# Optimization experiments

Measured on AMD Instinct MI355X. Metric: run time of the kernel, lower is better.

The kernel has to match this reference:

```python
import jax, jax.numpy as jnp
import numpy as np

N = 50000   # total nodes
E = 100000  # total edges
F = 64      # input node features
H = 128     # hidden_dim
HEADS = 4
B = 64      # number of graphs in the batch
S = 512     # num_stations
LC = 8      # num_line_colors


def setup_inputs() -> dict:
    key = jax.random.key(0)
    ks = jax.random.split(key, 40)
    w = lambda i, shape: (jax.random.normal(ks[i], shape, jnp.float32) * 0.02)
    inp = {
        'node_features': jax.random.normal(ks[0], (N, F), jnp.float32),
        'edge_index': jax.random.randint(ks[1], (2, E), 0, N),
        'batch': jnp.sort(jax.random.randint(ks[2], (N,), 0, B)),
        # initial projection F -> H
        'Wp': w(3, (F, H)), 'bp': w(4, (H,)),
        # TransformerConv 1: in H, out H, heads HEADS (concat)
        'Wq1': w(5, (H, HEADS * H)), 'bq1': w(6, (HEADS * H,)),
        'Wk1': w(7, (H, HEADS * H)), 'bk1': w(8, (HEADS * H,)),
        'Wv1': w(9, (H, HEADS * H)), 'bv1': w(10, (HEADS * H,)),
        'Ws1': w(11, (H, HEADS * H)), 'bs1': w(12, (HEADS * H,)),
        # TransformerConv 2: in HEADS*H, out H, heads 1
        'Wq2': w(13, (HEADS * H, H)), 'bq2': w(14, (H,)),
        'Wk2': w(15, (HEADS * H, H)), 'bk2': w(16, (H,)),
        'Wv2': w(17, (HEADS * H, H)), 'bv2': w(18, (H,)),
        'Ws2': w(19, (HEADS * H, H)), 'bs2': w(20, (H,)),
        # output heads
        'crW': w(21, (H, 1)),  'crb': w(22, (1,)),
        'hlW': w(23, (H, 4)),  'hlb': w(24, (4,)),
        'mtW': w(25, (H, 3)),  'mtb': w(26, (3,)),
        'p1W': w(27, (H, S)),  'p1b': w(28, (S,)),
        'p2W': w(29, (H, S)),  'p2b': w(30, (S,)),
        'dtW': w(31, (H, S)),  'dtb': w(32, (S,)),
        'slW': w(33, (H, LC)), 'slb': w(34, (LC,)),
    }
    return inp


def transformer_conv(x, src, dst, Wq, bq, Wk, bk, Wv, bv, Ws, bs, heads, out_ch):
    # PyG TransformerConv (beta=False, concat=True, root_weight=True):
    #   alpha_ij = softmax_j( (W_q x_i) . (W_k x_j) / sqrt(d) ) over in-edges of i
    #   out_i    = sum_j alpha_ij * (W_v x_j)  (concat heads) + W_skip x_i
    n = x.shape[0]
    q = (x @ Wq + bq).reshape(n, heads, out_ch)
    k = (x @ Wk + bk).reshape(n, heads, out_ch)
    v = (x @ Wv + bv).reshape(n, heads, out_ch)
    scores = jnp.sum(q[dst] * k[src], axis=-1) / jnp.sqrt(jnp.float32(out_ch))  # [E,heads]
    m = jax.ops.segment_max(scores, dst, num_segments=n)                        # per-target max
    e = jnp.exp(scores - m[dst])
    denom = jax.ops.segment_sum(e, dst, num_segments=n)
    alpha = e / (denom[dst] + 1e-16)                                            # [E,heads]
    out = jax.ops.segment_sum(alpha[:, :, None] * v[src], dst, num_segments=n)  # [N,heads,out]
    return out.reshape(n, heads * out_ch) + (x @ Ws + bs)


def reference(node_features, edge_index, batch, Wp, bp,
              Wq1, bq1, Wk1, bk1, Wv1, bv1, Ws1, bs1,
              Wq2, bq2, Wk2, bk2, Wv2, bv2, Ws2, bs2,
              crW, crb, hlW, hlb, mtW, mtb, p1W, p1b, p2W, p2b, dtW, dtb, slW, slb):
    src, dst = edge_index[0], edge_index[1]
    h = jax.nn.relu(node_features @ Wp + bp)
    h = jax.nn.relu(transformer_conv(h, src, dst, Wq1, bq1, Wk1, bk1, Wv1, bv1, Ws1, bs1, HEADS, H))
    h = jax.nn.relu(transformer_conv(h, src, dst, Wq2, bq2, Wk2, bk2, Wv2, bv2, Ws2, bs2, 1, H))
    # global mean pool over graphs
    counts = jax.ops.segment_sum(jnp.ones((h.shape[0],), h.dtype), batch, num_segments=B)
    g = jax.ops.segment_sum(h, batch, num_segments=B) / jnp.maximum(counts, 1.0)[:, None]  # [B,H]
    value = g @ crW + crb
    return (value,
            g @ hlW + hlb,
            g @ mtW + mtb,
            g @ p1W + p1b,
            g @ p2W + p2b,
            g @ dtW + dtb,
            g @ slW + slb)
```

## Files before the change

### kernel.cpp

```cpp
#include <hip/hip_runtime.h>
#include <hip/hip_bf16.h>

#define NN 50000
#define EE 100000
#define FF 64
#define HH 128
#define HEADS 4
#define BB 64
#define SS 512
#define LCC 8
#define DEGCAP 32

__device__ __forceinline__ float b2f(ushort u) {
    return __uint_as_float(((unsigned)u) << 16);
}
__device__ __forceinline__ ushort f2b(float f) {
    unsigned u = __float_as_uint(f);
    unsigned r = (u + 0x7FFFu + ((u >> 16) & 1u)) >> 16;
    return (ushort)r;
}
__device__ __forceinline__ uint f2b_pk(float a, float b) {
    __hip_bfloat162 h = __float22bfloat162_rn(make_float2(a, b));
    return *reinterpret_cast<uint*>(&h);
}

__device__ __forceinline__ uint f2fp8x4(float a, float b, float c, float d) {
    int r = __builtin_amdgcn_cvt_pk_fp8_f32(a, b, 0, false);
    r = __builtin_amdgcn_cvt_pk_fp8_f32(c, d, r, true);
    return (uint)r;
}
__device__ __forceinline__ void fp8x4(uint u, float* f) {
    auto lo = __builtin_amdgcn_cvt_pk_f32_fp8((int)u, false);
    auto hi = __builtin_amdgcn_cvt_pk_f32_fp8((int)u, true);
    f[0] = lo[0]; f[1] = lo[1]; f[2] = hi[0]; f[3] = hi[1];
}

typedef __attribute__((ext_vector_type(4))) float f32x4;
typedef __attribute__((ext_vector_type(8))) short s16x8;
typedef __attribute__((ext_vector_type(4))) uint u32x4;

__device__ __forceinline__ void glls16(const ushort* g, ushort* l) {
    __builtin_amdgcn_global_load_lds((const __attribute__((address_space(1))) void*)g,
                                     (__attribute__((address_space(3))) void*)l, 16, 0, 0);
}

#define BM 128
#define BN 128
#define BK 64
#define EST 68

__global__ __launch_bounds__(512) void gemm_wide(
    const ushort* __restrict__ A, const ushort* __restrict__ Bt,
    const float* __restrict__ bias,
    ushort* __restrict__ C1,
    unsigned char* __restrict__ D0, unsigned char* __restrict__ D1,
    unsigned char* __restrict__ D2,
    int mode, int M, int K, int gx, int gy)
{
    __shared__ __align__(16) ushort Sm[384 * 64];

    const int bid  = blockIdx.x;
    const int xcd  = bid & 7;
    const int slot = bid >> 3;
    const int bx   = slot % gx;
    const int by   = xcd + 8 * (slot / gx);
    if (by >= gy) return;
    const int m0 = by * BM;
    const int n0 = bx * 256;

    const int t = threadIdx.x;
    const int lane = t & 63;
    const int wave = t >> 6;
    const int wm = (wave & 1) * 64;
    const int wn = (wave >> 1) * 64;
    const int lrow = lane & 15;
    const int g    = lane >> 4;

    const int wbase = n0 + wn;
    float bj[4];
#pragma unroll
    for (int j = 0; j < 4; ++j) bj[j] = bias[wbase + j * 16 + lrow];

    const int scs = lane & 7;
    const ushort* gp[6];
#pragma unroll
    for (int p = 0; p < 6; ++p) {
        const int row = wave * 48 + p * 8 + (lane >> 3);
        const int l   = scs ^ (row & 7);
        gp[p] = (row < 128)
              ? A  + (size_t)min(m0 + row, M - 1) * K + (l << 3)
              : Bt + (size_t)(n0 + row - 128) * K + (l << 3);
    }

    f32x4 acc[4][4];
#pragma unroll
    for (int i = 0; i < 4; ++i)
#pragma unroll
        for (int j = 0; j < 4; ++j)
            acc[i][j] = (f32x4){bj[j], bj[j], bj[j], bj[j]};

    for (int k0 = 0; k0 < K; k0 += BK) {
#pragma unroll
        for (int p = 0; p < 6; ++p)
            glls16(gp[p] + k0, Sm + (wave * 48 + p * 8) * 64);
        __syncthreads();

#pragma unroll
        for (int kk = 0; kk < 2; ++kk) {
            s16x8 af[4], bf[4];
#pragma unroll
            for (int i = 0; i < 4; ++i) {
                const int R = wm + i * 16 + lrow;
                const int c = ((kk << 2) + g) ^ (R & 7);
                af[i] = *(const s16x8*)&Sm[(R << 6) + (c << 3)];
            }
#pragma unroll
            for (int j = 0; j < 4; ++j) {
                const int R = wn + j * 16 + lrow;
                const int c = ((kk << 2) + g) ^ (R & 7);
                bf[j] = *(const s16x8*)&Sm[((128 + R) << 6) + (c << 3)];
            }
#pragma unroll
            for (int i = 0; i < 4; ++i)
#pragma unroll
                for (int j = 0; j < 4; ++j)
                    acc[i][j] = __builtin_amdgcn_mfma_f32_16x16x32_bf16(af[i], bf[j], acc[i][j], 0, 0, 0);
        }
        __syncthreads();
    }

    float* Es = (float*)Sm + wave * (16 * EST);

    int dsel;
    ushort* Cw = C1; int ldw = 128; int cb = wbase;
    unsigned char* Cw8 = nullptr; int ldw8 = 0, cb8 = 0;
    if (mode == 1) {
        dsel = 1;
        if (wbase < 512) { Cw8 = D0; ldw8 = 512; cb8 = wbase; }
        else {
            const int u = wbase - 512;
            const int h = u >> 8;
            const int c = u & 255;
            if (c < 128) { Cw8 = D1; ldw8 = 512; cb8 = h * 128 + c; }
            else         { Cw8 = D2; ldw8 = 512; cb8 = h * 128 + (c - 128); }
        }
    } else {
        if (wbase < 128) { dsel = 0; }
        else { dsel = 1; Cw8 = D0; ldw8 = 384; cb8 = wbase - 128; }
    }

    const int rbase = (lane >> 4) * 4;
    const int rrow  = lane >> 2;
    const int rcol  = (lane & 3) << 4;

#pragma unroll
    for (int i = 0; i < 4; ++i) {
#pragma unroll
        for (int j = 0; j < 4; ++j)
#pragma unroll
            for (int r = 0; r < 4; ++r)
                Es[(rbase + r) * EST + j * 16 + lrow] = acc[i][j][r];
        const int gm = m0 + wm + i * 16 + rrow;
        if (gm < M) {
            const float* srcp = Es + rrow * EST + rcol;
            f32x4 f0 = *(const f32x4*)(srcp + 0);
            f32x4 f1 = *(const f32x4*)(srcp + 4);
            f32x4 f2 = *(const f32x4*)(srcp + 8);
            f32x4 f3 = *(const f32x4*)(srcp + 12);
            if (dsel == 0) {
                u32x4 o0, o1;
                o0[0] = f2b_pk(f0[0], f0[1]); o0[1] = f2b_pk(f0[2], f0[3]);
                o0[2] = f2b_pk(f1[0], f1[1]); o0[3] = f2b_pk(f1[2], f1[3]);
                o1[0] = f2b_pk(f2[0], f2[1]); o1[1] = f2b_pk(f2[2], f2[3]);
                o1[2] = f2b_pk(f3[0], f3[1]); o1[3] = f2b_pk(f3[2], f3[3]);
                ushort* dst = Cw + (size_t)gm * ldw + cb + rcol;
                *(u32x4*)(dst + 0) = o0;
                *(u32x4*)(dst + 8) = o1;
            } else {
                u32x4 o;
                o[0] = f2fp8x4(f0[0], f0[1], f0[2], f0[3]);
                o[1] = f2fp8x4(f1[0], f1[1], f1[2], f1[3]);
                o[2] = f2fp8x4(f2[0], f2[1], f2[2], f2[3]);
                o[3] = f2fp8x4(f3[0], f3[1], f3[2], f3[3]);
                *(u32x4*)(Cw8 + (size_t)gm * ldw8 + cb8 + rcol) = o;
            }
        }
    }
}

__global__ __launch_bounds__(256) void gemm_bf16(
    const ushort* __restrict__ A, const ushort* __restrict__ Bt,
    const float* __restrict__ bias,
    ushort* __restrict__ C1, int ld1,
    unsigned char* __restrict__ C2b,
    int M, int K, int relu, int gx, int gy)
{
    __shared__ __align__(16) ushort Sm[2 * BM * BK];
    ushort* As = Sm;
    ushort* Bs = Sm + BM * BK;

    const int bid  = blockIdx.x;
    const int xcd  = bid & 7;
    const int slot = bid >> 3;
    const int bx   = slot % gx;
    const int by   = xcd + 8 * (slot / gx);
    if (by >= gy) return;
    const int m0 = by * BM;
    const int n0 = bx * BN;

    const int t = threadIdx.x;
    const int lane = t & 63;
    const int wave = t >> 6;
    const int wm = (wave & 1) * 64;
    const int wn = (wave >> 1) * 64;
    const int lrow = lane & 15;
    const int g    = lane >> 4;

    const int wbase = n0 + wn;
    float bj[4];
#pragma unroll
    for (int j = 0; j < 4; ++j) bj[j] = bias[wbase + j * 16 + lrow];

    const int srow = (wave << 5) + (lane >> 3);
    const int scs  = lane & 7;

    const ushort* ga[4];
    const ushort* gb[4];
#pragma unroll
    for (int p = 0; p < 4; ++p) {
        const int row = srow + (p << 3);
        const int l   = scs ^ (row & 7);
        ga[p] = A + (size_t)min(m0 + row, M - 1) * K + (l << 3);
        gb[p] = Bt + (size_t)(n0 + row) * K + (l << 3);
    }
    const int ldsoff = (wave << 11);

    f32x4 acc[4][4];
#pragma unroll
    for (int i = 0; i < 4; ++i)
#pragma unroll
        for (int j = 0; j < 4; ++j)
            acc[i][j] = (f32x4){bj[j], bj[j], bj[j], bj[j]};

    for (int k0 = 0; k0 < K; k0 += BK) {
#pragma unroll
        for (int p = 0; p < 4; ++p) glls16(ga[p] + k0, As + ldsoff + (p << 9));
#pragma unroll
        for (int p = 0; p < 4; ++p) glls16(gb[p] + k0, Bs + ldsoff + (p << 9));
        __syncthreads();

#pragma unroll
        for (int kk = 0; kk < 2; ++kk) {
            s16x8 af[4], bf[4];
#pragma unroll
            for (int i = 0; i < 4; ++i) {
                const int R = wm + i * 16 + lrow;
                const int c = ((kk << 2) + g) ^ (R & 7);
                af[i] = *(const s16x8*)&As[(R << 6) + (c << 3)];
            }
#pragma unroll
            for (int j = 0; j < 4; ++j) {
                const int R = wn + j * 16 + lrow;
                const int c = ((kk << 2) + g) ^ (R & 7);
                bf[j] = *(const s16x8*)&Bs[(R << 6) + (c << 3)];
            }
#pragma unroll
            for (int i = 0; i < 4; ++i)
#pragma unroll
                for (int j = 0; j < 4; ++j)
                    acc[i][j] = __builtin_amdgcn_mfma_f32_16x16x32_bf16(af[i], bf[j], acc[i][j], 0, 0, 0);
        }
        __syncthreads();
    }

    float* Es = (float*)Sm + wave * (16 * EST);

    const int rbase = (lane >> 4) * 4;
    const int rrow  = lane >> 2;
    const int rcol  = (lane & 3) << 4;

#pragma unroll
    for (int i = 0; i < 4; ++i) {
#pragma unroll
        for (int j = 0; j < 4; ++j)
#pragma unroll
            for (int r = 0; r < 4; ++r) {
                float v = acc[i][j][r];
                if (relu) v = fmaxf(v, 0.f);
                Es[(rbase + r) * EST + j * 16 + lrow] = v;
            }
        const int gm = m0 + wm + i * 16 + rrow;
        if (gm < M) {
            const float* srcp = Es + rrow * EST + rcol;
            f32x4 f0 = *(const f32x4*)(srcp + 0);
            f32x4 f1 = *(const f32x4*)(srcp + 4);
            f32x4 f2 = *(const f32x4*)(srcp + 8);
            f32x4 f3 = *(const f32x4*)(srcp + 12);
            u32x4 o0, o1;
            o0[0] = f2b_pk(f0[0], f0[1]); o0[1] = f2b_pk(f0[2], f0[3]);
            o0[2] = f2b_pk(f1[0], f1[1]); o0[3] = f2b_pk(f1[2], f1[3]);
            o1[0] = f2b_pk(f2[0], f2[1]); o1[1] = f2b_pk(f2[2], f2[3]);
            o1[2] = f2b_pk(f3[0], f3[1]); o1[3] = f2b_pk(f3[2], f3[3]);
            ushort* dst = C1 + (size_t)gm * ld1 + wbase + rcol;
            *(u32x4*)(dst + 0) = o0;
            *(u32x4*)(dst + 8) = o1;
            u32x4 o;
            o[0] = f2fp8x4(16.f * f0[0], 16.f * f0[1], 16.f * f0[2], 16.f * f0[3]);
            o[1] = f2fp8x4(16.f * f1[0], 16.f * f1[1], 16.f * f1[2], 16.f * f1[3]);
            o[2] = f2fp8x4(16.f * f2[0], 16.f * f2[1], 16.f * f2[2], 16.f * f2[3]);
            o[3] = f2fp8x4(16.f * f3[0], 16.f * f3[1], 16.f * f3[2], 16.f * f3[3]);
            *(u32x4*)(C2b + (size_t)gm * 128 + wbase + rcol) = o;
        }
    }
}

#define F1OFF  8192
#define F2OFF  204800
#define WTOTAL 466944
#define BTOT   2048
#define MWORK  (HEADS * 128 * 128 + HEADS * 128)
#define CVTN   (NN * FF / 4)

__global__ void prep_kernel(
    const float* __restrict__ nf, ushort* __restrict__ nfb,
    const float* __restrict__ Wp,
    const float* __restrict__ Wq1, const float* __restrict__ Wk1,
    const float* __restrict__ Wv1, const float* __restrict__ Ws1,
    const float* __restrict__ Wq2, const float* __restrict__ Wk2,
    const float* __restrict__ Wv2, const float* __restrict__ Ws2,
    const float* __restrict__ bs1, const float* __restrict__ bq1,
    const float* __restrict__ bv1, const float* __restrict__ bs2,
    const float* __restrict__ bq2, const float* __restrict__ bk2, const float* __restrict__ bv2,
    ushort* __restrict__ wt, float* __restrict__ bb,
    unsigned* __restrict__ zerop, int zn)
{
    int t0 = blockIdx.x * 256 + threadIdx.x;
    if (t0 < CVTN) {
        float4 v = ((const float4*)nf)[t0];
        uint2 o;
        o.x = f2b_pk(v.x, v.y);
        o.y = f2b_pk(v.z, v.w);
        ((uint2*)nfb)[t0] = o;
        return;
    }
    int t = t0 - CVTN;
    if (t < WTOTAL) {
        float v;
        if (t < F1OFF) {
            int n = t >> 6, k = t & 63;
            v = Wp[k * 128 + n];
        } else if (t < F2OFF) {
            int u = t - F1OFF;
            int n = u >> 7, k = u & 127;
            if (n < 512) v = Ws1[k * 512 + n] * 16.0f;
            else {
                int r = n - 512;
                int h = r >> 8, c = r & 255;
                if (c < 128) return;
                v = Wv1[k * 512 + h * 128 + (c - 128)] * 16.0f;
            }
        } else {
            int u = t - F2OFF;
            int n = u >> 9, k = u & 511;
            if (n < 128) v = Ws2[k * 128 + n];
            else {
                int r = n - 128;
                const float* W = (r < 128) ? Wq2 : (r < 256) ? Wk2 : Wv2;
                v = W[k * 128 + (r & 127)] * 16.0f;
            }
        }
        wt[t] = f2b(v);
    } else if (t < WTOTAL + BTOT) {
        int u = t - WTOTAL;
        float v;
        if (u < 512) v = bs1[u] * 16.0f;
        else if (u < 1536) {
            int r = u - 512;
            int h = r >> 8, c = r & 255;
            if (c < 128) return;
            v = bv1[h * 128 + (c - 128)] * 16.0f;
        } else {
            int c = u - 1536;
            v = (c < 128) ? bs2[c]
              : (c < 256) ? bq2[c - 128] * 16.0f
              : (c < 384) ? bk2[c - 256] * 16.0f : bv2[c - 384] * 16.0f;
        }
        bb[u] = v;
    } else if (t < WTOTAL + BTOT + MWORK) {
        int m = t - (WTOTAL + BTOT);
        if (m < HEADS * 128 * 128) {
            int h = m >> 14;
            int rem = m & 16383;
            int b = rem >> 7, a = rem & 127;
            const float* wq = Wq1 + a * 512 + h * 128;
            const float* wk = Wk1 + b * 512 + h * 128;
            float acc = 0.f;
#pragma unroll 8
            for (int d = 0; d < 128; ++d) acc += wq[d] * wk[d];
            wt[F1OFF + (size_t)(512 + h * 256 + b) * 128 + a] = f2b(acc * 16.0f);
        } else {
            int u = m - HEADS * 128 * 128;
            int h = u >> 7, b = u & 127;
            const float* wk = Wk1 + b * 512 + h * 128;
            const float* bq = bq1 + h * 128;
            float acc = 0.f;
#pragma unroll 8
            for (int d = 0; d < 128; ++d) acc += wk[d] * bq[d];
            bb[512 + h * 256 + b] = acc * 16.0f;
        }
    } else {
        int z = t - (WTOTAL + BTOT + MWORK);
        if (z < zn) zerop[z] = 0u;
    }
}

__global__ void bucket_direct_kernel(const int* __restrict__ src, const int* __restrict__ dst,
                                     int* __restrict__ cnt, int* __restrict__ srcs2, int E)
{
    int e = blockIdx.x * 256 + threadIdx.x;
    if (e >= E) return;
    int d = dst[e];
    int p = atomicAdd(&cnt[d], 1);
    if (p < DEGCAP) srcs2[d * DEGCAP + p] = src[e];
}

__global__ __launch_bounds__(256) void gather4_kernel(
    const unsigned char* __restrict__ Qu, const unsigned char* __restrict__ kq8,
    const unsigned char* __restrict__ v4,
    const int* __restrict__ cnt, const int* __restrict__ srcs2,
    const unsigned char* __restrict__ s8,
    ushort* __restrict__ outp, float scale, int n)
{
    int i = blockIdx.x * 4 + (threadIdx.x >> 6);
    int lane = threadIdx.x & 63;
    if (i >= n) return;
    const int h = lane >> 4;
    const int l = lane & 15;
    const int vo = h * 128 + l * 8;

    uint2 uq = *(const uint2*)(Qu + (size_t)i * 512 + h * 128 + l * 8);
    uint2 sk = *(const uint2*)(s8 + (size_t)i * 512 + h * 128 + l * 8);
    float q[8];
    fp8x4(uq.x, q); fp8x4(uq.y, q + 4);

    const int deg = min(cnt[i], DEGCAP);
    const int* rowp = srcs2 + (size_t)i * DEGCAP;
    float den = 0.f;
    float o[8] = {0.f, 0.f, 0.f, 0.f, 0.f, 0.f, 0.f, 0.f};
    int p = 0;
    for (; p + 2 <= deg; p += 2) {
        int s0 = rowp[p], s1 = rowp[p + 1];
        uint2 ka = *(const uint2*)(kq8 + (size_t)s0 * 128 + l * 8);
        uint2 kb = *(const uint2*)(kq8 + (size_t)s1 * 128 + l * 8);
        uint2 va = *(const uint2*)(v4 + (size_t)s0 * 512 + vo);
        uint2 vb = *(const uint2*)(v4 + (size_t)s1 * 512 + vo);
        float kaf[8], kbf[8];
        fp8x4(ka.x, kaf); fp8x4(ka.y, kaf + 4);
        fp8x4(kb.x, kbf); fp8x4(kb.y, kbf + 4);
        float da = 0.f, db = 0.f;
#pragma unroll
        for (int d = 0; d < 8; ++d) {
            da += q[d] * kaf[d];
            db += q[d] * kbf[d];
        }
#pragma unroll
        for (int off = 8; off > 0; off >>= 1) {
            da += __shfl_xor(da, off, 64);
            db += __shfl_xor(db, off, 64);
        }
        float ea = __expf(da * scale);
        float eb = __expf(db * scale);
        den += ea + eb;
        float fa[8], fb[8];
        fp8x4(va.x, fa); fp8x4(va.y, fa + 4);
        fp8x4(vb.x, fb); fp8x4(vb.y, fb + 4);
#pragma unroll
        for (int d = 0; d < 8; ++d) o[d] += ea * fa[d] + eb * fb[d];
    }
    if (p < deg) {
        int s = rowp[p];
        uint2 kv = *(const uint2*)(kq8 + (size_t)s * 128 + l * 8);
        uint2 vv = *(const uint2*)(v4 + (size_t)s * 512 + vo);
        float kf[8];
        fp8x4(kv.x, kf); fp8x4(kv.y, kf + 4);
        float d0 = 0.f;
#pragma unroll
        for (int d = 0; d < 8; ++d) d0 += q[d] * kf[d];
#pragma unroll
        for (int off = 8; off > 0; off >>= 1) d0 += __shfl_xor(d0, off, 64);
        float e = __expf(d0 * scale);
        den += e;
        float fv[8];
        fp8x4(vv.x, fv); fp8x4(vv.y, fv + 4);
#pragma unroll
        for (int d = 0; d < 8; ++d) o[d] += e * fv[d];
    }
    float invd = 1.0f / (den + 1e-16f);
    float skf[8];
    fp8x4(sk.x, skf); fp8x4(sk.y, skf + 4);
    float r[8];
#pragma unroll
    for (int d = 0; d < 8; ++d) r[d] = 0.0625f * fmaxf(skf[d] + o[d] * invd, 0.f);
    u32x4 ov;
    ov[0] = f2b_pk(r[0], r[1]);
    ov[1] = f2b_pk(r[2], r[3]);
    ov[2] = f2b_pk(r[4], r[5]);
    ov[3] = f2b_pk(r[6], r[7]);
    *(u32x4*)(outp + (size_t)i * 512 + h * 128 + l * 8) = ov;
}

__global__ __launch_bounds__(256) void edge_gather_kernel(
    const unsigned char* __restrict__ qkv,
    const int* __restrict__ cnt, const int* __restrict__ srcs2,
    const ushort* __restrict__ skip,
    ushort* __restrict__ outp, float scale, int n)
{
    int i = blockIdx.x * 4 + (threadIdx.x >> 6);
    int lane = threadIdx.x & 63;
    if (i >= n) return;
    const int g = lane >> 4;
    const int l = lane & 15;

    uint2 uq = *(const uint2*)(qkv + (size_t)i * 384 + l * 8);
    float q[8];
    fp8x4(uq.x, q); fp8x4(uq.y, q + 4);

    const int deg = min(cnt[i], DEGCAP);
    const int* rowp = srcs2 + (size_t)i * DEGCAP;
    float den = 0.f;
    float o[8] = {0.f, 0.f, 0.f, 0.f, 0.f, 0.f, 0.f, 0.f};
    for (int pb = 0; pb < deg; pb += 4) {
        int p = pb + g;
        bool act = p < deg;
        int s = rowp[act ? p : 0];
        const unsigned char* row = qkv + (size_t)s * 384;
        uint2 kv = *(const uint2*)(row + 128 + l * 8);
        uint2 vv = *(const uint2*)(row + 256 + l * 8);
        float kf[8];
        fp8x4(kv.x, kf); fp8x4(kv.y, kf + 4);
        float d0 = 0.f;
#pragma unroll
        for (int d = 0; d < 8; ++d) d0 += q[d] * kf[d];
#pragma unroll
        for (int off = 8; off > 0; off >>= 1) d0 += __shfl_xor(d0, off, 64);
        float e = act ? __expf(d0 * scale) : 0.f;
        den += e;
        float vf[8];
        fp8x4(vv.x, vf); fp8x4(vv.y, vf + 4);
#pragma unroll
        for (int d = 0; d < 8; ++d) o[d] += e * vf[d];
    }
#pragma unroll
    for (int off = 16; off < 64; off <<= 1) {
        den += __shfl_xor(den, off, 64);
#pragma unroll
        for (int d = 0; d < 8; ++d) o[d] += __shfl_xor(o[d], off, 64);
    }
    if (g == 0) {
        float inv = 0.0625f / (den + 1e-16f);
        s16x8 sk = *(const s16x8*)(skip + (size_t)i * 128 + l * 8);
        float r[8];
// ... 72 lines not shown
                              hipStream_t stream)
{
    (void)in_sizes; (void)n_in; (void)out_size; (void)ws_size;

    const float* nf   = (const float*)d_in[0];
    const int*   ei   = (const int*)d_in[1];
    const int*   src  = ei;
    const int*   dst  = ei + EE;
    const int*   batch= (const int*)d_in[2];
    const float* Wp   = (const float*)d_in[3];
    const float* bp   = (const float*)d_in[4];
    const float* Wq1  = (const float*)d_in[5];
    const float* bq1  = (const float*)d_in[6];
    const float* Wk1  = (const float*)d_in[7];
    const float* bk1  = (const float*)d_in[8];
    const float* Wv1  = (const float*)d_in[9];
    const float* bv1  = (const float*)d_in[10];
    const float* Ws1  = (const float*)d_in[11];
    const float* bs1  = (const float*)d_in[12];
    const float* Wq2  = (const float*)d_in[13];
    const float* bq2  = (const float*)d_in[14];
    const float* Wk2  = (const float*)d_in[15];
    const float* bk2  = (const float*)d_in[16];
    const float* Wv2  = (const float*)d_in[17];
    const float* bv2  = (const float*)d_in[18];
    const float* Ws2  = (const float*)d_in[19];
    const float* bs2  = (const float*)d_in[20];
    const float* crW  = (const float*)d_in[21];
    const float* crb  = (const float*)d_in[22];
    const float* hlW  = (const float*)d_in[23];
    const float* hlb  = (const float*)d_in[24];
    const float* mtW  = (const float*)d_in[25];
    const float* mtb  = (const float*)d_in[26];
    const float* p1W  = (const float*)d_in[27];
    const float* p1b  = (const float*)d_in[28];
    const float* p2W  = (const float*)d_in[29];
    const float* p2b  = (const float*)d_in[30];
    const float* dtW  = (const float*)d_in[31];
    const float* dtb  = (const float*)d_in[32];
    const float* slW  = (const float*)d_in[33];
    const float* slb  = (const float*)d_in[34];
    float* out = (float*)d_out;

    (void)bk1;

    unsigned char* base = (unsigned char*)d_ws;
    unsigned char* kq8 = base;
    unsigned char* v4  = base + (size_t)NN * 128;
    unsigned char* Qu8 = base + (size_t)NN * 640;
    ushort* h2sb = (ushort*)base;
    unsigned char* qkv8 = base + (size_t)NN * 256;
    ushort* h2   = (ushort*)(base + (size_t)NN * 640);
    unsigned char* s8 = base + (size_t)NN * 1152;
    ushort* h0b  = (ushort*)(base + (size_t)NN * 1664);
    ushort* h1b  = (ushort*)(base + (size_t)NN * 1920);
    ushort* nfb  = h1b;
    ushort* wt   = (ushort*)(base + (size_t)NN * 2944);
    float*  bb   = (float*)(wt + WTOTAL);
    int*    srcs2 = (int*)(bb + BTOT);
    int*    cnt   = srcs2 + (size_t)NN * DEGCAP;
    float*  gsum  = (float*)(cnt + NN);
    float*  cntb  = gsum + BB * HH;

    const float scale = 0.08838834764831845f;
    const dim3 blk(256);
    const int gy  = (NN + BM - 1) / BM;
    const int gyp = ((gy + 7) / 8) * 8;

    const int filln = NN + BB * HH + BB;
    const int ptot = CVTN + WTOTAL + BTOT + MWORK + filln;
    prep_kernel<<<(ptot + 255) / 256, blk, 0, stream>>>(
        nf, nfb, Wp, Wq1, Wk1, Wv1, Ws1, Wq2, Wk2, Wv2, Ws2,
        bs1, bq1, bv1, bs2, bq2, bk2, bv2, wt, bb, (unsigned*)cnt, filln);

    bucket_direct_kernel<<<(EE + 255) / 256, blk, 0, stream>>>(src, dst, cnt, srcs2, EE);

    gemm_bf16<<<dim3(1 * gyp), blk, 0, stream>>>(
        nfb, wt, bp, h0b, HH, kq8, NN, FF, 1, 1, gy);

    gemm_wide<<<dim3(6 * gyp), dim3(512), 0, stream>>>(
        h0b, wt + F1OFF, bb, nullptr, s8, Qu8, v4, 1, NN, HH, 6, gy);

    gather4_kernel<<<(NN + 3) / 4, blk, 0, stream>>>(
        Qu8, kq8, v4, cnt, srcs2, s8, h1b, scale * 0.00390625f, NN);

    gemm_wide<<<dim3(2 * gyp), dim3(512), 0, stream>>>(
        h1b, wt + F2OFF, bb + 1536, h2sb, qkv8, nullptr, nullptr, 2, NN, 4 * HH, 2, gy);

    edge_gather_kernel<<<(NN + 3) / 4, blk, 0, stream>>>(
        qkv8, cnt, srcs2, h2sb, h2, scale * 0.00390625f, NN);

    pool_kernel<<<(NN + 255) / 256, blk, 0, stream>>>(h2, batch, gsum, cntb, NN);

    const int total = BB * (1 + 4 + 3 + SS + SS + SS + LCC);
    out_heads_kernel<<<(total + 255) / 256, blk, 0, stream>>>(
        gsum, cntb, crW, crb, hlW, hlb, mtW, mtb, p1W, p1b, p2W, p2b, dtW, dtb, slW, slb, out, total);
}
```

Before: 321.1 us.

## Run second-layer projection GEMM in FP8 with FP8 layer-1 activations

The layer-1 gather now writes its output in FP8 instead of BF16. The second projection GEMM moves into a new kernel, gemm_f2, that uses FP8 MFMA on FP8 weights prepared in prep_kernel, with the scale factors folded into the bias and the epilogue. This halves the bytes of the 50000x512 activation written and read back, and uses the faster FP8 matrix instructions. The cost is lower precision in both activations and weights, which risks accuracy against tolerance.

```diff
diff --git a/kernel.cpp b/kernel.cpp
--- a/kernel.cpp
+++ b/kernel.cpp
@@ -34,12 +34,20 @@
     auto hi = __builtin_amdgcn_cvt_pk_f32_fp8((int)u, true);
     f[0] = lo[0]; f[1] = lo[1]; f[2] = hi[0]; f[3] = hi[1];
 }
+__device__ __forceinline__ unsigned char f2fp8_1(float v) {
+    int r = __builtin_amdgcn_cvt_pk_fp8_f32(v, 0.f, 0, false);
+    return (unsigned char)(r & 0xFF);
+}
 
 typedef __attribute__((ext_vector_type(4))) float f32x4;
 typedef __attribute__((ext_vector_type(8))) short s16x8;
 typedef __attribute__((ext_vector_type(4))) uint u32x4;
 
 __device__ __forceinline__ void glls16(const ushort* g, ushort* l) {
+    __builtin_amdgcn_global_load_lds((const __attribute__((address_space(1))) void*)g,
+                                     (__attribute__((address_space(3))) void*)l, 16, 0, 0);
+}
+__device__ __forceinline__ void glls16b(const unsigned char* g, unsigned char* l) {
     __builtin_amdgcn_global_load_lds((const __attribute__((address_space(1))) void*)g,
                                      (__attribute__((address_space(3))) void*)l, 16, 0, 0);
 }
@@ -52,10 +60,9 @@
 __global__ __launch_bounds__(512) void gemm_wide(
     const ushort* __restrict__ A, const ushort* __restrict__ Bt,
     const float* __restrict__ bias,
-    ushort* __restrict__ C1,
     unsigned char* __restrict__ D0, unsigned char* __restrict__ D1,
     unsigned char* __restrict__ D2,
-    int mode, int M, int K, int gx, int gy)
+    int M, int K, int gx, int gy)
 {
     __shared__ __align__(16) ushort Sm[384 * 64];
 
@@ -131,22 +138,14 @@
 
     float* Es = (float*)Sm + wave * (16 * EST);
 
-    int dsel;
-    ushort* Cw = C1; int ldw = 128; int cb = wbase;
-    unsigned char* Cw8 = nullptr; int ldw8 = 0, cb8 = 0;
-    if (mode == 1) {
-        dsel = 1;
-        if (wbase < 512) { Cw8 = D0; ldw8 = 512; cb8 = wbase; }
-        else {
-            const int u = wbase - 512;
-            const int h = u >> 8;
-            const int c = u & 255;
-            if (c < 128) { Cw8 = D1; ldw8 = 512; cb8 = h * 128 + c; }
-            else         { Cw8 = D2; ldw8 = 512; cb8 = h * 128 + (c - 128); }
-        }
-    } else {
-        if (wbase < 128) { dsel = 0; }
-        else { dsel = 1; Cw8 = D0; ldw8 = 384; cb8 = wbase - 128; }
+    unsigned char* Cw8; int ldw8, cb8;
+    if (wbase < 512) { Cw8 = D0; ldw8 = 512; cb8 = wbase; }
+    else {
+        const int u = wbase - 512;
+        const int h = u >> 8;
+        const int c = u & 255;
+        if (c < 128) { Cw8 = D1; ldw8 = 512; cb8 = h * 128 + c; }
+        else         { Cw8 = D2; ldw8 = 512; cb8 = h * 128 + (c - 128); }
     }
 
     const int rbase = (lane >> 4) * 4;
@@ -167,13 +166,123 @@
             f32x4 f1 = *(const f32x4*)(srcp + 4);
             f32x4 f2 = *(const f32x4*)(srcp + 8);
             f32x4 f3 = *(const f32x4*)(srcp + 12);
-            if (dsel == 0) {
+            u32x4 o;
+            o[0] = f2fp8x4(f0[0], f0[1], f0[2], f0[3]);
+            o[1] = f2fp8x4(f1[0], f1[1], f1[2], f1[3]);
+            o[2] = f2fp8x4(f2[0], f2[1], f2[2], f2[3]);
+            o[3] = f2fp8x4(f3[0], f3[1], f3[2], f3[3]);
+            *(u32x4*)(Cw8 + (size_t)gm * ldw8 + cb8 + rcol) = o;
+        }
+    }
+}
+
+__global__ __launch_bounds__(512) void gemm_f2(
+    const unsigned char* __restrict__ A8, const unsigned char* __restrict__ B8,
+    const float* __restrict__ bias,
+    ushort* __restrict__ h2sb, unsigned char* __restrict__ qkv8,
+    int M, int gy)
+{
+    __shared__ __align__(16) unsigned char Sm[384 * 128];
+
+    const int bid  = blockIdx.x;
+    const int xcd  = bid & 7;
+    const int slot = bid >> 3;
+    const int bx   = slot % 2;
+    const int by   = xcd + 8 * (slot / 2);
+    if (by >= gy) return;
+    const int m0 = by * BM;
+    const int n0 = bx * 256;
+
+    const int t = threadIdx.x;
+    const int lane = t & 63;
+    const int wave = t >> 6;
+    const int wm = (wave & 1) * 64;
+    const int wn = (wave >> 1) * 64;
+    const int lrow = lane & 15;
+    const int g    = lane >> 4;
+
+    const int wbase = n0 + wn;
+    float bj[4];
+#pragma unroll
+    for (int j = 0; j < 4; ++j) bj[j] = bias[wbase + j * 16 + lrow];
+
+    const unsigned char* gp[6];
+#pragma unroll
+    for (int p = 0; p < 6; ++p) {
+        const int row = wave * 48 + p * 8 + (lane >> 3);
+        const int cg  = ((lane & 7) ^ (row & 7)) << 4;
+        gp[p] = (row < 128)
+              ? A8 + (size_t)min(m0 + row, M - 1) * 512 + cg
+              : B8 + (size_t)(n0 + row - 128) * 512 + cg;
+    }
+
+    f32x4 acc[4][4];
+#pragma unroll
+    for (int i = 0; i < 4; ++i)
+#pragma unroll
+        for (int j = 0; j < 4; ++j)
+            acc[i][j] = (f32x4){bj[j], bj[j], bj[j], bj[j]};
+
+    const int sub = ((g & 1) << 3);
+    for (int k0 = 0; k0 < 512; k0 += 128) {
+#pragma unroll
+        for (int p = 0; p < 6; ++p)
+            glls16b(gp[p] + k0, Sm + (wave * 48 + p * 8) * 128);
+        __syncthreads();
+
+#pragma unroll
+        for (int kk = 0; kk < 4; ++kk) {
+            const int gr = (kk << 1) + (g >> 1);
+            long af[4], bf[4];
+#pragma unroll
+            for (int i = 0; i < 4; ++i) {
+                const int R = wm + i * 16 + lrow;
+                af[i] = *(const long*)&Sm[(R << 7) + ((gr ^ (R & 7)) << 4) + sub];
+            }
+#pragma unroll
+            for (int j = 0; j < 4; ++j) {
+                const int R = wn + j * 16 + lrow;
+                bf[j] = *(const long*)&Sm[((128 + R) << 7) + ((gr ^ (R & 7)) << 4) + sub];
+            }
+#pragma unroll
+            for (int i = 0; i < 4; ++i)
+#pragma unroll
+                for (int j = 0; j < 4; ++j)
+                    acc[i][j] = __builtin_amdgcn_mfma_f32_16x16x32_fp8_fp8(af[i], bf[j], acc[i][j], 0, 0, 0);
+        }
+        __syncthreads();
+    }
+
+    float* Es = (float*)Sm + wave * (16 * EST);
+
+    const bool skipw = (wbase < 128);
+    const float os = skipw ? (1.0f / 256.0f) : 0.0625f;
+
+    const int rbase = (lane >> 4) * 4;
+    const int rrow  = lane >> 2;
+    const int rcol  = (lane & 3) << 4;
+
+#pragma unroll
+    for (int i = 0; i < 4; ++i) {
+#pragma unroll
+        for (int j = 0; j < 4; ++j)
+#pragma unroll
+            for (int r = 0; r < 4; ++r)
+                Es[(rbase + r) * EST + j * 16 + lrow] = acc[i][j][r] * os;
+        const int gm = m0 + wm + i * 16 + rrow;
+        if (gm < M) {
+            const float* srcp = Es + rrow * EST + rcol;
+            f32x4 f0 = *(const f32x4*)(srcp + 0);
+            f32x4 f1 = *(const f32x4*)(srcp + 4);
+            f32x4 f2 = *(const f32x4*)(srcp + 8);
+            f32x4 f3 = *(const f32x4*)(srcp + 12);
+            if (skipw) {
                 u32x4 o0, o1;
                 o0[0] = f2b_pk(f0[0], f0[1]); o0[1] = f2b_pk(f0[2], f0[3]);
                 o0[2] = f2b_pk(f1[0], f1[1]); o0[3] = f2b_pk(f1[2], f1[3]);
                 o1[0] = f2b_pk(f2[0], f2[1]); o1[1] = f2b_pk(f2[2], f2[3]);
                 o1[2] = f2b_pk(f3[0], f3[1]); o1[3] = f2b_pk(f3[2], f3[3]);
-                ushort* dst = Cw + (size_t)gm * ldw + cb + rcol;
+                ushort* dst = h2sb + (size_t)gm * 128 + wbase + rcol;
                 *(u32x4*)(dst + 0) = o0;
                 *(u32x4*)(dst + 8) = o1;
             } else {
@@ -182,7 +291,7 @@
                 o[1] = f2fp8x4(f1[0], f1[1], f1[2], f1[3]);
                 o[2] = f2fp8x4(f2[0], f2[1], f2[2], f2[3]);
                 o[3] = f2fp8x4(f3[0], f3[1], f3[2], f3[3]);
-                *(u32x4*)(Cw8 + (size_t)gm * ldw8 + cb8 + rcol) = o;
+                *(u32x4*)(qkv8 + (size_t)gm * 384 + (wbase - 128) + rcol) = o;
             }
         }
     }
@@ -331,7 +440,7 @@
     const float* __restrict__ bs1, const float* __restrict__ bq1,
     const float* __restrict__ bv1, const float* __restrict__ bs2,
     const float* __restrict__ bq2, const float* __restrict__ bk2, const float* __restrict__ bv2,
-    ushort* __restrict__ wt, float* __restrict__ bb,
+    ushort* __restrict__ wt, unsigned char* __restrict__ f2w8, float* __restrict__ bb,
     unsigned* __restrict__ zerop, int zn)
 {
     int t0 = blockIdx.x * 256 + threadIdx.x;
@@ -362,12 +471,15 @@
         } else {
             int u = t - F2OFF;
             int n = u >> 9, k = u & 511;
-            if (n < 128) v = Ws2[k * 128 + n];
+            float w;
+            if (n < 128) w = Ws2[k * 128 + n];
             else {
                 int r = n - 128;
                 const float* W = (r < 128) ? Wq2 : (r < 256) ? Wk2 : Wv2;
-                v = W[k * 128 + (r & 127)] * 16.0f;
-            }
+                w = W[k * 128 + (r & 127)];
+            }
+            f2w8[(size_t)n * 512 + k] = f2fp8_1(w * 16.0f);
+            return;
         }
         wt[t] = f2b(v);
     } else if (t < WTOTAL + BTOT) {
@@ -381,9 +493,9 @@
             v = bv1[h * 128 + (c - 128)] * 16.0f;
         } else {
             int c = u - 1536;
-            v = (c < 128) ? bs2[c]
-              : (c < 256) ? bq2[c - 128] * 16.0f
-              : (c < 384) ? bk2[c - 256] * 16.0f : bv2[c - 384] * 16.0f;
+            v = 256.0f * ((c < 128) ? bs2[c]
+              : (c < 256) ? bq2[c - 128]
+              : (c < 384) ? bk2[c - 256] : bv2[c - 384]);
         }
         bb[u] = v;
     } else if (t < WTOTAL + BTOT + MWORK) {
@@ -429,7 +541,7 @@
     const unsigned char* __restrict__ v4,
     const int* __restrict__ cnt, const int* __restrict__ srcs2,
     const unsigned char* __restrict__ s8,
-    ushort* __restrict__ outp, float scale, int n)
+    unsigned char* __restrict__ outp, float scale, int n)
 {
     int i = blockIdx.x * 4 + (threadIdx.x >> 6);
     int lane = threadIdx.x & 63;
@@ -500,13 +612,11 @@
     fp8x4(sk.x, skf); fp8x4(sk.y, skf + 4);
     float r[8];
 #pragma unroll
-    for (int d = 0; d < 8; ++d) r[d] = 0.0625f * fmaxf(skf[d] + o[d] * invd, 0.f);
-    u32x4 ov;
-    ov[0] = f2b_pk(r[0], r[1]);
-    ov[1] = f2b_pk(r[2], r[3]);
-    ov[2] = f2b_pk(r[4], r[5]);
-    ov[3] = f2b_pk(r[6], r[7]);
-    *(u32x4*)(outp + (size_t)i * 512 + h * 128 + l * 8) = ov;
+    for (int d = 0; d < 8; ++d) r[d] = fmaxf(skf[d] + o[d] * invd, 0.f);
+    uint2 ov;
+    ov.x = f2fp8x4(r[0], r[1], r[2], r[3]);
+    ov.y = f2fp8x4(r[4], r[5], r[6], r[7]);
+    *(uint2*)(outp + (size_t)i * 512 + h * 128 + l * 8) = ov;
 }
 
 __global__ __launch_bounds__(256) void edge_gather_kernel(
@@ -686,11 +796,12 @@
     ushort* h2   = (ushort*)(base + (size_t)NN * 640);
     unsigned char* s8 = base + (size_t)NN * 1152;
     ushort* h0b  = (ushort*)(base + (size_t)NN * 1664);
-    ushort* h1b  = (ushort*)(base + (size_t)NN * 1920);
-    ushort* nfb  = h1b;
-    ushort* wt   = (ushort*)(base + (size_t)NN * 2944);
-    float*  bb   = (float*)(wt + WTOTAL);
-    int*    srcs2 = (int*)(bb + BTOT);
+    unsigned char* h1f8 = base + (size_t)NN * 1920;
+    ushort* nfb  = (ushort*)h1f8;
+    ushort* wt   = (ushort*)(base + (size_t)NN * 2432);
+    float*  bb   = (float*)(wt + F2OFF);
+    unsigned char* f2w8 = (unsigned char*)(bb + BTOT);
+    int*    srcs2 = (int*)(f2w8 + 512 * 512);
     int*    cnt   = srcs2 + (size_t)NN * DEGCAP;
     float*  gsum  = (float*)(cnt + NN);
     float*  cntb  = gsum + BB * HH;
@@ -704,7 +815,7 @@
     const int ptot = CVTN + WTOTAL + BTOT + MWORK + filln;
     prep_kernel<<<(ptot + 255) / 256, blk, 0, stream>>>(
         nf, nfb, Wp, Wq1, Wk1, Wv1, Ws1, Wq2, Wk2, Wv2, Ws2,
-        bs1, bq1, bv1, bs2, bq2, bk2, bv2, wt, bb, (unsigned*)cnt, filln);
+        bs1, bq1, bv1, bs2, bq2, bk2, bv2, wt, f2w8, bb, (unsigned*)cnt, filln);
 
     bucket_direct_kernel<<<(EE + 255) / 256, blk, 0, stream>>>(src, dst, cnt, srcs2, EE);
 
@@ -712,13 +823,13 @@
         nfb, wt, bp, h0b, HH, kq8, NN, FF, 1, 1, gy);
 
     gemm_wide<<<dim3(6 * gyp), dim3(512), 0, stream>>>(
-        h0b, wt + F1OFF, bb, nullptr, s8, Qu8, v4, 1, NN, HH, 6, gy);
+        h0b, wt + F1OFF, bb, s8, Qu8, v4, NN, HH, 6, gy);
 
     gather4_kernel<<<(NN + 3) / 4, blk, 0, stream>>>(
-        Qu8, kq8, v4, cnt, srcs2, s8, h1b, scale * 0.00390625f, NN);
-
-    gemm_wide<<<dim3(2 * gyp), dim3(512), 0, stream>>>(
-        h1b, wt + F2OFF, bb + 1536, h2sb, qkv8, nullptr, nullptr, 2, NN, 4 * HH, 2, gy);
+        Qu8, kq8, v4, cnt, srcs2, s8, h1f8, scale * 0.00390625f, NN);
+
+    gemm_f2<<<dim3(2 * gyp), dim3(512), 0, stream>>>(
+        h1f8, f2w8, bb + 1536, h2sb, qkv8, NN, gy);
 
     edge_gather_kernel<<<(NN + 3) / 4, blk, 0, stream>>>(
         qkv8, cnt, srcs2, h2sb, h2, scale * 0.00390625f, NN);
```

Result: faster. 306.8 us (-4.5%).

## Switch wide GEMMs to FP8 MFMA with FP8 activations and weights

Applied to the files above, without the earlier changes.

Converts both wide projection GEMMs from bf16 to fp8 inputs using the 16x16x32 fp8 MFMA, with weights pre-quantized to fp8 and bias and output scales adjusted. The first projection now writes only fp8 output, dropping its bf16 store, and the layer-1 gather emits fp8 instead of bf16. This halves activation and weight bytes loaded and written between stages and doubles K per LDS tile. The cost is extra quantization error from fp8 activations into the second layer.

```diff
diff --git a/kernel.cpp b/kernel.cpp
--- a/kernel.cpp
+++ b/kernel.cpp
@@ -34,12 +34,20 @@
     auto hi = __builtin_amdgcn_cvt_pk_f32_fp8((int)u, true);
     f[0] = lo[0]; f[1] = lo[1]; f[2] = hi[0]; f[3] = hi[1];
 }
+__device__ __forceinline__ unsigned char f2fp8_1(float v) {
+    int r = __builtin_amdgcn_cvt_pk_fp8_f32(v, 0.f, 0, false);
+    return (unsigned char)(r & 0xFF);
+}
 
 typedef __attribute__((ext_vector_type(4))) float f32x4;
 typedef __attribute__((ext_vector_type(8))) short s16x8;
 typedef __attribute__((ext_vector_type(4))) uint u32x4;
 
 __device__ __forceinline__ void glls16(const ushort* g, ushort* l) {
+    __builtin_amdgcn_global_load_lds((const __attribute__((address_space(1))) void*)g,
+                                     (__attribute__((address_space(3))) void*)l, 16, 0, 0);
+}
+__device__ __forceinline__ void glls16b(const unsigned char* g, unsigned char* l) {
     __builtin_amdgcn_global_load_lds((const __attribute__((address_space(1))) void*)g,
                                      (__attribute__((address_space(3))) void*)l, 16, 0, 0);
 }
@@ -49,15 +57,15 @@
 #define BK 64
 #define EST 68
 
-__global__ __launch_bounds__(512) void gemm_wide(
-    const ushort* __restrict__ A, const ushort* __restrict__ Bt,
+__global__ __launch_bounds__(512) void gemm_f8(
+    const unsigned char* __restrict__ A8, const unsigned char* __restrict__ B8,
     const float* __restrict__ bias,
     ushort* __restrict__ C1,
     unsigned char* __restrict__ D0, unsigned char* __restrict__ D1,
     unsigned char* __restrict__ D2,
     int mode, int M, int K, int gx, int gy)
 {
-    __shared__ __align__(16) ushort Sm[384 * 64];
+    __shared__ __align__(16) unsigned char Sm[384 * 128];
 
     const int bid  = blockIdx.x;
     const int xcd  = bid & 7;
@@ -81,15 +89,14 @@
 #pragma unroll
     for (int j = 0; j < 4; ++j) bj[j] = bias[wbase + j * 16 + lrow];
 
-    const int scs = lane & 7;
-    const ushort* gp[6];
+    const unsigned char* gp[6];
 #pragma unroll
     for (int p = 0; p < 6; ++p) {
         const int row = wave * 48 + p * 8 + (lane >> 3);
-        const int l   = scs ^ (row & 7);
+        const int cg  = ((lane & 7) ^ (row & 7)) << 4;
         gp[p] = (row < 128)
-              ? A  + (size_t)min(m0 + row, M - 1) * K + (l << 3)
-              : Bt + (size_t)(n0 + row - 128) * K + (l << 3);
+              ? A8 + (size_t)min(m0 + row, M - 1) * K + cg
+              : B8 + (size_t)(n0 + row - 128) * K + cg;
     }
 
     f32x4 acc[4][4];
@@ -99,43 +106,42 @@
         for (int j = 0; j < 4; ++j)
             acc[i][j] = (f32x4){bj[j], bj[j], bj[j], bj[j]};
 
-    for (int k0 = 0; k0 < K; k0 += BK) {
+    const int sub = ((g & 1) << 3);
+    for (int k0 = 0; k0 < K; k0 += 128) {
 #pragma unroll
         for (int p = 0; p < 6; ++p)
-            glls16(gp[p] + k0, Sm + (wave * 48 + p * 8) * 64);
+            glls16b(gp[p] + k0, Sm + (wave * 48 + p * 8) * 128);
         __syncthreads();
 
 #pragma unroll
-        for (int kk = 0; kk < 2; ++kk) {
-            s16x8 af[4], bf[4];
+        for (int kk = 0; kk < 4; ++kk) {
+            const int gr = (kk << 1) + (g >> 1);
+            long af[4], bf[4];
 #pragma unroll
             for (int i = 0; i < 4; ++i) {
                 const int R = wm + i * 16 + lrow;
-                const int c = ((kk << 2) + g) ^ (R & 7);
-                af[i] = *(const s16x8*)&Sm[(R << 6) + (c << 3)];
+                af[i] = *(const long*)&Sm[(R << 7) + ((gr ^ (R & 7)) << 4) + sub];
             }
 #pragma unroll
             for (int j = 0; j < 4; ++j) {
                 const int R = wn + j * 16 + lrow;
-                const int c = ((kk << 2) + g) ^ (R & 7);
-                bf[j] = *(const s16x8*)&Sm[((128 + R) << 6) + (c << 3)];
+                bf[j] = *(const long*)&Sm[((128 + R) << 7) + ((gr ^ (R & 7)) << 4) + sub];
             }
 #pragma unroll
             for (int i = 0; i < 4; ++i)
 #pragma unroll
                 for (int j = 0; j < 4; ++j)
-                    acc[i][j] = __builtin_amdgcn_mfma_f32_16x16x32_bf16(af[i], bf[j], acc[i][j], 0, 0, 0);
+                    acc[i][j] = __builtin_amdgcn_mfma_f32_16x16x32_fp8_fp8(af[i], bf[j], acc[i][j], 0, 0, 0);
         }
         __syncthreads();
     }
 
     float* Es = (float*)Sm + wave * (16 * EST);
 
-    int dsel;
-    ushort* Cw = C1; int ldw = 128; int cb = wbase;
+    bool bfout = false;
+    float os = 0.0625f;
     unsigned char* Cw8 = nullptr; int ldw8 = 0, cb8 = 0;
     if (mode == 1) {
-        dsel = 1;
         if (wbase < 512) { Cw8 = D0; ldw8 = 512; cb8 = wbase; }
         else {
             const int u = wbase - 512;
@@ -145,8 +151,8 @@
             else         { Cw8 = D2; ldw8 = 512; cb8 = h * 128 + (c - 128); }
         }
     } else {
-        if (wbase < 128) { dsel = 0; }
-        else { dsel = 1; Cw8 = D0; ldw8 = 384; cb8 = wbase - 128; }
+        if (wbase < 128) { bfout = true; os = 1.0f / 256.0f; }
+        else { Cw8 = D0; ldw8 = 384; cb8 = wbase - 128; }
     }
 
     const int rbase = (lane >> 4) * 4;
@@ -159,7 +165,7 @@
         for (int j = 0; j < 4; ++j)
 #pragma unroll
             for (int r = 0; r < 4; ++r)
-                Es[(rbase + r) * EST + j * 16 + lrow] = acc[i][j][r];
+                Es[(rbase + r) * EST + j * 16 + lrow] = acc[i][j][r] * os;
         const int gm = m0 + wm + i * 16 + rrow;
         if (gm < M) {
             const float* srcp = Es + rrow * EST + rcol;
@@ -167,13 +173,13 @@
             f32x4 f1 = *(const f32x4*)(srcp + 4);
             f32x4 f2 = *(const f32x4*)(srcp + 8);
             f32x4 f3 = *(const f32x4*)(srcp + 12);
-            if (dsel == 0) {
+            if (bfout) {
                 u32x4 o0, o1;
                 o0[0] = f2b_pk(f0[0], f0[1]); o0[1] = f2b_pk(f0[2], f0[3]);
                 o0[2] = f2b_pk(f1[0], f1[1]); o0[3] = f2b_pk(f1[2], f1[3]);
                 o1[0] = f2b_pk(f2[0], f2[1]); o1[1] = f2b_pk(f2[2], f2[3]);
                 o1[2] = f2b_pk(f3[0], f3[1]); o1[3] = f2b_pk(f3[2], f3[3]);
-                ushort* dst = Cw + (size_t)gm * ldw + cb + rcol;
+                ushort* dst = C1 + (size_t)gm * 128 + wbase + rcol;
                 *(u32x4*)(dst + 0) = o0;
                 *(u32x4*)(dst + 8) = o1;
             } else {
@@ -191,9 +197,8 @@
 __global__ __launch_bounds__(256) void gemm_bf16(
     const ushort* __restrict__ A, const ushort* __restrict__ Bt,
     const float* __restrict__ bias,
-    ushort* __restrict__ C1, int ld1,
-    unsigned char* __restrict__ C2b,
-    int M, int K, int relu, int gx, int gy)
+    unsigned char* __restrict__ C8,
+    int M, int K, int gy)
 {
     __shared__ __align__(16) ushort Sm[2 * BM * BK];
     ushort* As = Sm;
@@ -201,12 +206,9 @@
 
     const int bid  = blockIdx.x;
     const int xcd  = bid & 7;
-    const int slot = bid >> 3;
-    const int bx   = slot % gx;
-    const int by   = xcd + 8 * (slot / gx);
+    const int by   = xcd + 8 * (bid >> 3);
     if (by >= gy) return;
     const int m0 = by * BM;
-    const int n0 = bx * BN;
 
     const int t = threadIdx.x;
     const int lane = t & 63;
@@ -216,7 +218,7 @@
     const int lrow = lane & 15;
     const int g    = lane >> 4;
 
-    const int wbase = n0 + wn;
+    const int wbase = wn;
     float bj[4];
 #pragma unroll
     for (int j = 0; j < 4; ++j) bj[j] = bias[wbase + j * 16 + lrow];
@@ -231,7 +233,7 @@
         const int row = srow + (p << 3);
         const int l   = scs ^ (row & 7);
         ga[p] = A + (size_t)min(m0 + row, M - 1) * K + (l << 3);
-        gb[p] = Bt + (size_t)(n0 + row) * K + (l << 3);
+        gb[p] = Bt + (size_t)row * K + (l << 3);
     }
     const int ldsoff = (wave << 11);
 
@@ -284,11 +286,8 @@
 #pragma unroll
         for (int j = 0; j < 4; ++j)
 #pragma unroll
-            for (int r = 0; r < 4; ++r) {
-                float v = acc[i][j][r];
-                if (relu) v = fmaxf(v, 0.f);
-                Es[(rbase + r) * EST + j * 16 + lrow] = v;
-            }
+            for (int r = 0; r < 4; ++r)
+                Es[(rbase + r) * EST + j * 16 + lrow] = fmaxf(acc[i][j][r], 0.f);
         const int gm = m0 + wm + i * 16 + rrow;
         if (gm < M) {
             const float* srcp = Es + rrow * EST + rcol;
@@ -296,20 +295,12 @@
             f32x4 f1 = *(const f32x4*)(srcp + 4);
             f32x4 f2 = *(const f32x4*)(srcp + 8);
             f32x4 f3 = *(const f32x4*)(srcp + 12);
-            u32x4 o0, o1;
-            o0[0] = f2b_pk(f0[0], f0[1]); o0[1] = f2b_pk(f0[2], f0[3]);
-            o0[2] = f2b_pk(f1[0], f1[1]); o0[3] = f2b_pk(f1[2], f1[3]);
-            o1[0] = f2b_pk(f2[0], f2[1]); o1[1] = f2b_pk(f2[2], f2[3]);
-            o1[2] = f2b_pk(f3[0], f3[1]); o1[3] = f2b_pk(f3[2], f3[3]);
-            ushort* dst = C1 + (size_t)gm * ld1 + wbase + rcol;
-            *(u32x4*)(dst + 0) = o0;
-            *(u32x4*)(dst + 8) = o1;
             u32x4 o;
             o[0] = f2fp8x4(16.f * f0[0], 16.f * f0[1], 16.f * f0[2], 16.f * f0[3]);
             o[1] = f2fp8x4(16.f * f1[0], 16.f * f1[1], 16.f * f1[2], 16.f * f1[3]);
             o[2] = f2fp8x4(16.f * f2[0], 16.f * f2[1], 16.f * f2[2], 16.f * f2[3]);
             o[3] = f2fp8x4(16.f * f3[0], 16.f * f3[1], 16.f * f3[2], 16.f * f3[3]);
-            *(u32x4*)(C2b + (size_t)gm * 128 + wbase + rcol) = o;
+            *(u32x4*)(C8 + (size_t)gm * 128 + wbase + rcol) = o;
         }
     }
 }
@@ -331,7 +322,8 @@
     const float* __restrict__ bs1, const float* __restrict__ bq1,
     const float* __restrict__ bv1, const float* __restrict__ bs2,
     const float* __restrict__ bq2, const float* __restrict__ bk2, const float* __restrict__ bv2,
-    ushort* __restrict__ wt, float* __restrict__ bb,
+    ushort* __restrict__ wt, unsigned char* __restrict__ f1w8, unsigned char* __restrict__ f2w8,
+    float* __restrict__ bb,
     unsigned* __restrict__ zerop, int zn)
 {
     int t0 = blockIdx.x * 256 + threadIdx.x;
@@ -345,45 +337,47 @@
     }
     int t = t0 - CVTN;
     if (t < WTOTAL) {
-        float v;
         if (t < F1OFF) {
             int n = t >> 6, k = t & 63;
-            v = Wp[k * 128 + n];
+            wt[t] = f2b(Wp[k * 128 + n]);
         } else if (t < F2OFF) {
             int u = t - F1OFF;
             int n = u >> 7, k = u & 127;
-            if (n < 512) v = Ws1[k * 512 + n] * 16.0f;
+            float v;
+            if (n < 512) v = Ws1[k * 512 + n];
             else {
                 int r = n - 512;
                 int h = r >> 8, c = r & 255;
                 if (c < 128) return;
-                v = Wv1[k * 512 + h * 128 + (c - 128)] * 16.0f;
+                v = Wv1[k * 512 + h * 128 + (c - 128)];
             }
+            f1w8[(size_t)n * 128 + k] = f2fp8_1(v * 16.0f);
         } else {
             int u = t - F2OFF;
             int n = u >> 9, k = u & 511;
-            if (n < 128) v = Ws2[k * 128 + n];
+            float w;
+            if (n < 128) w = Ws2[k * 128 + n];
             else {
                 int r = n - 128;
                 const float* W = (r < 128) ? Wq2 : (r < 256) ? Wk2 : Wv2;
-                v = W[k * 128 + (r & 127)] * 16.0f;
+                w = W[k * 128 + (r & 127)];
             }
-        }
-        wt[t] = f2b(v);
+            f2w8[(size_t)n * 512 + k] = f2fp8_1(w * 16.0f);
+        }
     } else if (t < WTOTAL + BTOT) {
         int u = t - WTOTAL;
         float v;
-        if (u < 512) v = bs1[u] * 16.0f;
+        if (u < 512) v = bs1[u] * 256.0f;
         else if (u < 1536) {
             int r = u - 512;
             int h = r >> 8, c = r & 255;
             if (c < 128) return;
-            v = bv1[h * 128 + (c - 128)] * 16.0f;
+            v = bv1[h * 128 + (c - 128)] * 256.0f;
         } else {
             int c = u - 1536;
-            v = (c < 128) ? bs2[c]
-              : (c < 256) ? bq2[c - 128] * 16.0f
-              : (c < 384) ? bk2[c - 256] * 16.0f : bv2[c - 384] * 16.0f;
+            v = 256.0f * ((c < 128) ? bs2[c]
+              : (c < 256) ? bq2[c - 128]
+              : (c < 384) ? bk2[c - 256] : bv2[c - 384]);
         }
         bb[u] = v;
     } else if (t < WTOTAL + BTOT + MWORK) {
@@ -397,7 +391,7 @@
             float acc = 0.f;
 #pragma unroll 8
             for (int d = 0; d < 128; ++d) acc += wq[d] * wk[d];
-            wt[F1OFF + (size_t)(512 + h * 256 + b) * 128 + a] = f2b(acc * 16.0f);
+            f1w8[(size_t)(512 + h * 256 + b) * 128 + a] = f2fp8_1(acc * 16.0f);
         } else {
             int u = m - HEADS * 128 * 128;
             int h = u >> 7, b = u & 127;
@@ -406,7 +400,7 @@
             float acc = 0.f;
 #pragma unroll 8
             for (int d = 0; d < 128; ++d) acc += wk[d] * bq[d];
-            bb[512 + h * 256 + b] = acc * 16.0f;
+            bb[512 + h * 256 + b] = acc * 256.0f;
         }
     } else {
         int z = t - (WTOTAL + BTOT + MWORK);
@@ -429,7 +423,7 @@
     const unsigned char* __restrict__ v4,
     const int* __restrict__ cnt, const int* __restrict__ srcs2,
     const unsigned char* __restrict__ s8,
-    ushort* __restrict__ outp, float scale, int n)
+    unsigned char* __restrict__ outp, float scale, int n)
 {
     int i = blockIdx.x * 4 + (threadIdx.x >> 6);
     int lane = threadIdx.x & 63;
@@ -500,13 +494,11 @@
     fp8x4(sk.x, skf); fp8x4(sk.y, skf + 4);
     float r[8];
 #pragma unroll
-    for (int d = 0; d < 8; ++d) r[d] = 0.0625f * fmaxf(skf[d] + o[d] * invd, 0.f);
-    u32x4 ov;
-    ov[0] = f2b_pk(r[0], r[1]);
-    ov[1] = f2b_pk(r[2], r[3]);
-    ov[2] = f2b_pk(r[4], r[5]);
-    ov[3] = f2b_pk(r[6], r[7]);
-    *(u32x4*)(outp + (size_t)i * 512 + h * 128 + l * 8) = ov;
+    for (int d = 0; d < 8; ++d) r[d] = fmaxf(skf[d] + o[d] * invd, 0.f);
+    uint2 ov;
+    ov.x = f2fp8x4(r[0], r[1], r[2], r[3]);
+    ov.y = f2fp8x4(r[4], r[5], r[6], r[7]);
+    *(uint2*)(outp + (size_t)i * 512 + h * 128 + l * 8) = ov;
 }
 
 __global__ __launch_bounds__(256) void edge_gather_kernel(
@@ -685,12 +677,13 @@
     unsigned char* qkv8 = base + (size_t)NN * 256;
     ushort* h2   = (ushort*)(base + (size_t)NN * 640);
     unsigned char* s8 = base + (size_t)NN * 1152;
-    ushort* h0b  = (ushort*)(base + (size_t)NN * 1664);
-    ushort* h1b  = (ushort*)(base + (size_t)NN * 1920);
-    ushort* nfb  = h1b;
-    ushort* wt   = (ushort*)(base + (size_t)NN * 2944);
-    float*  bb   = (float*)(wt + WTOTAL);
-    int*    srcs2 = (int*)(bb + BTOT);
+    unsigned char* h1f8 = base + (size_t)NN * 1664;
+    ushort* nfb  = (ushort*)h1f8;
+    ushort* wt   = (ushort*)(base + (size_t)NN * 2176);
+    float*  bb   = (float*)(wt + F1OFF);
+    unsigned char* f1w8 = (unsigned char*)(bb + BTOT);
+    unsigned char* f2w8 = f1w8 + 1536 * 128;
+    int*    srcs2 = (int*)(f2w8 + 512 * 512);
     int*    cnt   = srcs2 + (size_t)NN * DEGCAP;
     float*  gsum  = (float*)(cnt + NN);
     float*  cntb  = gsum + BB * HH;
@@ -704,21 +697,21 @@
     const int ptot = CVTN + WTOTAL + BTOT + MWORK + filln;
     prep_kernel<<<(ptot + 255) / 256, blk, 0, stream>>>(
         nf, nfb, Wp, Wq1, Wk1, Wv1, Ws1, Wq2, Wk2, Wv2, Ws2,
-        bs1, bq1, bv1, bs2, bq2, bk2, bv2, wt, bb, (unsigned*)cnt, filln);
+        bs1, bq1, bv1, bs2, bq2, bk2, bv2, wt, f1w8, f2w8, bb, (unsigned*)cnt, filln);
 
     bucket_direct_kernel<<<(EE + 255) / 256, blk, 0, stream>>>(src, dst, cnt, srcs2, EE);
 
-    gemm_bf16<<<dim3(1 * gyp), blk, 0, stream>>>(
-        nfb, wt, bp, h0b, HH, kq8, NN, FF, 1, 1, gy);
-
-    gemm_wide<<<dim3(6 * gyp), dim3(512), 0, stream>>>(
-        h0b, wt + F1OFF, bb, nullptr, s8, Qu8, v4, 1, NN, HH, 6, gy);
+    gemm_bf16<<<dim3(gyp), blk, 0, stream>>>(
+        nfb, wt, bp, kq8, NN, FF, gy);
+
+    gemm_f8<<<dim3(6 * gyp), dim3(512), 0, stream>>>(
+        kq8, f1w8, bb, nullptr, s8, Qu8, v4, 1, NN, 128, 6, gy);
 
     gather4_kernel<<<(NN + 3) / 4, blk, 0, stream>>>(
-        Qu8, kq8, v4, cnt, srcs2, s8, h1b, scale * 0.00390625f, NN);
-
-    gemm_wide<<<dim3(2 * gyp), dim3(512), 0, stream>>>(
-        h1b, wt + F2OFF, bb + 1536, h2sb, qkv8, nullptr, nullptr, 2, NN, 4 * HH, 2, gy);
+        Qu8, kq8, v4, cnt, srcs2, s8, h1f8, scale * 0.00390625f, NN);
+
+    gemm_f8<<<dim3(2 * gyp), dim3(512), 0, stream>>>(
+        h1f8, f2w8, bb + 1536, h2sb, qkv8, nullptr, nullptr, 2, NN, 512, 2, gy);
 
     edge_gather_kernel<<<(NN + 3) / 4, blk, 0, stream>>>(
         qkv8, cnt, srcs2, h2sb, h2, scale * 0.00390625f, NN);
```

After: 299.6 us. 1.07x faster.
